# Optimization experiments

Hardware: AMD Instinct MI355X
Metric: run time of the kernel (lower is better)

The kernel has to match this reference:

```python
import jax, jax.numpy as jnp
import numpy as np

N_NODES = 50000
N_EDGES = 500000
HIDDEN = 64
NUM_BASIS = 32
NUM_SH = 4  # (lmax+1)^2 with lmax=1


def _mlp(x, w1, b1, w2, b2):
    # Linear -> SiLU -> Linear, matching nn.Sequential(Linear, SiLU, Linear)
    return jax.nn.silu(x @ w1 + b1) @ w2 + b2


def setup_inputs() -> dict:
    key = jax.random.key(0)
    ks = jax.random.split(key, 10)
    scale_in = 1.0 / np.sqrt(NUM_BASIS)
    scale_h = 1.0 / np.sqrt(HIDDEN)
    return {
        "scalar": jax.random.normal(ks[0], (N_NODES, HIDDEN), dtype=jnp.float32),
        "vector": jax.random.normal(ks[1], (N_NODES, 3, HIDDEN), dtype=jnp.float32),
        "edge_sh": jax.random.normal(ks[2], (N_EDGES, NUM_SH), dtype=jnp.float32),
        "edge_length": jax.random.uniform(ks[3], (N_EDGES, NUM_BASIS), dtype=jnp.float32),
        "edge_index": jax.random.randint(ks[4], (2, N_EDGES), 0, N_NODES, dtype=jnp.int32),
        "sw1": jax.random.normal(ks[5], (NUM_BASIS, HIDDEN), dtype=jnp.float32) * scale_in,
        "sb1": jnp.zeros((HIDDEN,), dtype=jnp.float32),
        "sw2": jax.random.normal(ks[6], (HIDDEN, HIDDEN), dtype=jnp.float32) * scale_h,
        "sb2": jnp.zeros((HIDDEN,), dtype=jnp.float32),
        "vw1": jax.random.normal(ks[7], (NUM_BASIS, HIDDEN), dtype=jnp.float32) * scale_in,
        "vb1": jnp.zeros((HIDDEN,), dtype=jnp.float32),
        "vw2": jax.random.normal(ks[8], (HIDDEN, HIDDEN), dtype=jnp.float32) * scale_h,
        "vb2": jnp.zeros((HIDDEN,), dtype=jnp.float32),
    }


def reference(scalar, vector, edge_sh, edge_length, edge_index,
              sw1, sb1, sw2, sb2, vw1, vb1, vw2, vb2):
    # edge_sh is accepted (as in the torch forward signature) but unused.
    row, col = edge_index[0], edge_index[1]
    n = scalar.shape[0]

    # Edge-wise MLP weights from radial basis expansion: [E, hidden]
    scalar_weights = _mlp(edge_length, sw1, sb1, sw2, sb2)
    # Gather source-node scalars, weight, scatter-add to destination nodes.
    scalar_msg = scalar[col] * scalar_weights                   # [E, hidden]
    out_scalar = jax.ops.segment_sum(scalar_msg, row, num_segments=n)

    vector_weights = _mlp(edge_length, vw1, vb1, vw2, vb2)      # [E, hidden]
    vector_msg = vector[col] * vector_weights[:, None, :]       # [E, 3, hidden]
    out_vector = jax.ops.segment_sum(vector_msg, row, num_segments=n)

    return out_scalar, out_vector
```

## Files before the change

kernel.cpp:

```cpp
#include <hip/hip_runtime.h>

#define HIDDEN 64
#define NB 32
#define SCAN_BLOCK 1024
#define HSTR 72

typedef __attribute__((ext_vector_type(8))) short bf16x8;
typedef __attribute__((ext_vector_type(4))) float f32x4;

static __device__ __forceinline__ unsigned short f2bf(float x) {
    union { float f; unsigned u; } v; v.f = x;
    unsigned r = v.u + 0x7fffu + ((v.u >> 16) & 1u);
    return (unsigned short)(r >> 16);
}
static __device__ __forceinline__ float bf2f(unsigned short s) {
    union { unsigned u; float f; } v; v.u = ((unsigned)s) << 16;
    return v.f;
}

__global__ __launch_bounds__(256) void hist_kernel(
    const int* __restrict__ edge_index, int* __restrict__ counts, int E)
{
    int i = blockIdx.x * 256 + threadIdx.x;
    if (i < E) atomicAdd(&counts[edge_index[i]], 1);
}

__global__ __launch_bounds__(SCAN_BLOCK) void scan_pass1(
    const int* __restrict__ counts, int* __restrict__ partial,
    int* __restrict__ blocksums, int N)
{
    __shared__ int tmp[SCAN_BLOCK];
    const int t = threadIdx.x;
    const int gid = blockIdx.x * SCAN_BLOCK + t;
    int v = (gid < N) ? counts[gid] : 0;
    tmp[t] = v;
    __syncthreads();
    for (int off = 1; off < SCAN_BLOCK; off <<= 1) {
        int x = (t >= off) ? tmp[t - off] : 0;
        __syncthreads();
        tmp[t] += x;
        __syncthreads();
    }
    if (gid < N) partial[gid] = tmp[t] - v;
    if (t == SCAN_BLOCK - 1) blocksums[blockIdx.x] = tmp[t];
}

__global__ void scan_pass2(int* __restrict__ blocksums, int nb)
{
    if (threadIdx.x == 0) {
        int acc = 0;
        for (int i = 0; i < nb; ++i) { int v = blocksums[i]; blocksums[i] = acc; acc += v; }
    }
}

__global__ __launch_bounds__(SCAN_BLOCK) void scan_pass3(
    const int* __restrict__ partial, const int* __restrict__ blocksums,
    int* __restrict__ offsets, int* __restrict__ cursors, int N, int E)
{
    const int gid = blockIdx.x * SCAN_BLOCK + threadIdx.x;
    if (gid < N) {
        int o = partial[gid] + blocksums[blockIdx.x];
        offsets[gid] = o;
        cursors[gid] = o;
    }
    if (blockIdx.x == 0 && threadIdx.x == 0) offsets[N] = E;
}

__global__ __launch_bounds__(256) void scatter_kernel(
    const int* __restrict__ edge_index, int* __restrict__ cursors,
    int* __restrict__ perm, int* __restrict__ perm_col, int E)
{
    int i = blockIdx.x * 256 + threadIdx.x;
    if (i < E) {
        int pos = atomicAdd(&cursors[edge_index[i]], 1);
        perm[pos] = i;
        perm_col[pos] = edge_index[E + i];
    }
}

__global__ __launch_bounds__(256) void mlp_mfma_kernel(
    const float* __restrict__ edge_length,
    const int*   __restrict__ perm,
    const float* __restrict__ sw1, const float* __restrict__ sb1,
    const float* __restrict__ sw2, const float* __restrict__ sb2,
    const float* __restrict__ vw1, const float* __restrict__ vb1,
    const float* __restrict__ vw2, const float* __restrict__ vb2,
    unsigned short* __restrict__ Ws,
    unsigned short* __restrict__ Wv,
    int E, int nchunks)
{
    __shared__ short Hs[4][64 * HSTR];

    const int t    = threadIdx.x;
    const int lane = t & 63;
    const int wid  = t >> 6;
    const int quad = lane >> 4;
    const int l16  = lane & 15;
    short* Hw = Hs[wid];

    const float* w1p[2] = {sw1, vw1};
    const float* b1p[2] = {sb1, vb1};
    const float* w2p[2] = {sw2, vw2};
    const float* b2p[2] = {sb2, vb2};
    unsigned short* outp[2] = {Ws, Wv};

    bf16x8 w1f[2][4];
    bf16x8 w2f[2][2][4];
    float  b1v[2][4], b2v[2][4];
    #pragma unroll
    for (int m = 0; m < 2; ++m) {
        #pragma unroll
        for (int nt = 0; nt < 4; ++nt) {
            const int col = nt * 16 + l16;
            #pragma unroll
            for (int j = 0; j < 8; ++j)
                w1f[m][nt][j] = (short)f2bf(w1p[m][(quad * 8 + j) * HIDDEN + col]);
            #pragma unroll
            for (int kk = 0; kk < 2; ++kk) {
                #pragma unroll
                for (int j = 0; j < 8; ++j)
                    w2f[m][kk][nt][j] = (short)f2bf(w2p[m][(kk * 32 + quad * 8 + j) * HIDDEN + col]);
            }
            b1v[m][nt] = b1p[m][col];
            b2v[m][nt] = b2p[m][col];
        }
    }

    const int wave_g = blockIdx.x * 4 + wid;
    const int nwaves = gridDim.x * 4;

    for (int c = wave_g; c < nchunks; c += nwaves) {
        const int j0 = c * 64;

        bf16x8 af[4];
        #pragma unroll
        for (int mt = 0; mt < 4; ++mt) {
            int j = j0 + mt * 16 + l16;
            int e = perm[j < E ? j : (E - 1)];
            const float* r = edge_length + (size_t)e * NB + quad * 8;
            float4 u0 = *(const float4*)r;
            float4 u1 = *(const float4*)(r + 4);
            af[mt][0] = (short)f2bf(u0.x); af[mt][1] = (short)f2bf(u0.y);
            af[mt][2] = (short)f2bf(u0.z); af[mt][3] = (short)f2bf(u0.w);
            af[mt][4] = (short)f2bf(u1.x); af[mt][5] = (short)f2bf(u1.y);
            af[mt][6] = (short)f2bf(u1.z); af[mt][7] = (short)f2bf(u1.w);
        }

        #pragma unroll
        for (int m = 0; m < 2; ++m) {
            #pragma unroll
            for (int mt = 0; mt < 4; ++mt) {
                #pragma unroll
                for (int nt = 0; nt < 4; ++nt) {
                    f32x4 cf = {b1v[m][nt], b1v[m][nt], b1v[m][nt], b1v[m][nt]};
                    cf = __builtin_amdgcn_mfma_f32_16x16x32_bf16(af[mt], w1f[m][nt], cf, 0, 0, 0);
                    #pragma unroll
                    for (int r4 = 0; r4 < 4; ++r4) {
                        float x = cf[r4];
                        x = x / (1.0f + __expf(-x));
                        const int row = mt * 16 + quad * 4 + r4;
                        Hw[row * HSTR + nt * 16 + l16] = (short)f2bf(x);
                    }
                }
            }

            #pragma unroll
            for (int mt = 0; mt < 4; ++mt) {
                const int arow = mt * 16 + l16;
                bf16x8 a0 = *(const bf16x8*)(Hw + arow * HSTR + quad * 8);
                bf16x8 a1 = *(const bf16x8*)(Hw + arow * HSTR + 32 + quad * 8);
                #pragma unroll
                for (int nt = 0; nt < 4; ++nt) {
                    f32x4 cf = {b2v[m][nt], b2v[m][nt], b2v[m][nt], b2v[m][nt]};
                    cf = __builtin_amdgcn_mfma_f32_16x16x32_bf16(a1, w2f[m][1][nt], cf, 0, 0, 0);
                    cf = __builtin_amdgcn_mfma_f32_16x16x32_bf16(a0, w2f[m][0][nt], cf, 0, 0, 0);
                    #pragma unroll
                    for (int r4 = 0; r4 < 4; ++r4) {
                        const int row = mt * 16 + quad * 4 + r4;
                        Hw[row * HSTR + nt * 16 + l16] = (short)f2bf(cf[r4]);
                    }
                }
            }

            unsigned short* op = outp[m] + (size_t)j0 * HIDDEN;
            #pragma unroll
            for (int i = 0; i < 8; ++i) {
                const int row = i * 8 + (lane >> 3);
                bf16x8 v = *(const bf16x8*)(Hw + row * HSTR + (lane & 7) * 8);
                if (j0 + row < E)
                    *(bf16x8*)(op + (size_t)i * 512 + lane * 8) = v;
            }
        }
    }
}

__global__ __launch_bounds__(256) void node_kernel(
    const float* __restrict__ scalar,
    const float* __restrict__ vector,
    const int* __restrict__ offsets,
    const int* __restrict__ perm_col,
    const unsigned short* __restrict__ Ws,
    const unsigned short* __restrict__ Wv,
    float* __restrict__ out_scalar,
    float* __restrict__ out_vector,
    int N)
{
    const int lane = threadIdx.x & 63;
    const int wave = blockIdx.x * 4 + (threadIdx.x >> 6);
    const int nw   = gridDim.x * 4;

    for (int n = wave; n < N; n += nw) {
        const int beg = offsets[n];
        const int end = offsets[n + 1];

        float as = 0.0f, a0 = 0.0f, a1 = 0.0f, a2 = 0.0f;

        for (int j = beg; j < end; ++j) {
            const int col = perm_col[j];
            const float w_s = bf2f(Ws[(size_t)j * HIDDEN + lane]);
            const float w_v = bf2f(Wv[(size_t)j * HIDDEN + lane]);
            const float* sp = scalar + (size_t)col * HIDDEN;
            const float* vp = vector + (size_t)col * 3 * HIDDEN;
            as = fmaf(sp[lane],       w_s, as);
            a0 = fmaf(vp[lane],       w_v, a0);
            a1 = fmaf(vp[64 + lane],  w_v, a1);
            a2 = fmaf(vp[128 + lane], w_v, a2);
        }

        out_scalar[(size_t)n * HIDDEN + lane] = as;
        float* ov = out_vector + (size_t)n * 3 * HIDDEN;
        ov[lane]       = a0;
        ov[64 + lane]  = a1;
        ov[128 + lane] = a2;
    }
}

extern "C" void kernel_launch(void* const* d_in, const int* in_sizes, int n_in,
                              void* d_out, int out_size, void* d_ws, size_t ws_size,
                              hipStream_t stream) {
    const float* scalar      = (const float*)d_in[0];
    const float* vector      = (const float*)d_in[1];
    const float* edge_length = (const float*)d_in[3];
    const int*   edge_index  = (const int*)d_in[4];
    const float* sw1 = (const float*)d_in[5];
    const float* sb1 = (const float*)d_in[6];
    const float* sw2 = (const float*)d_in[7];
    const float* sb2 = (const float*)d_in[8];
    const float* vw1 = (const float*)d_in[9];
    const float* vb1 = (const float*)d_in[10];
    const float* vw2 = (const float*)d_in[11];
    const float* vb2 = (const float*)d_in[12];

    const int N = in_sizes[0] / HIDDEN;
    const int E = in_sizes[4] / 2;

    float* out_scalar = (float*)d_out;
    float* out_vector = (float*)d_out + (size_t)N * HIDDEN;

    unsigned short* Ws = (unsigned short*)d_ws;
    unsigned short* Wv = Ws + (size_t)E * HIDDEN;
    int* ib = (int*)((char*)d_ws + (size_t)E * HIDDEN * 2 * 2);
    int* counts    = ib;
    int* partial   = ib + N;
    int* offsets   = ib + 2 * N;
    int* cursors   = ib + 3 * N + 1;
    int* blocksums = ib + 4 * N + 1;
    int* perm      = ib + 4 * N + 1 + 64;
    int* perm_col  = perm + E;

    hipMemsetAsync(counts, 0, (size_t)N * sizeof(int), stream);

    const int egrid = (E + 255) / 256;
    hist_kernel<<<egrid, 256, 0, stream>>>(edge_index, counts, E);

    const int nb = (N + SCAN_BLOCK - 1) / SCAN_BLOCK;
    scan_pass1<<<nb, SCAN_BLOCK, 0, stream>>>(counts, partial, blocksums, N);
    scan_pass2<<<1, 64, 0, stream>>>(blocksums, nb);
    scan_pass3<<<nb, SCAN_BLOCK, 0, stream>>>(partial, blocksums, offsets, cursors, N, E);

    scatter_kernel<<<egrid, 256, 0, stream>>>(edge_index, cursors, perm, perm_col, E);

    const int nchunks = (E + 63) / 64;
    mlp_mfma_kernel<<<512, 256, 0, stream>>>(
        edge_length, perm,
        sw1, sb1, sw2, sb2, vw1, vb1, vw2, vb2,
        Ws, Wv, E, nchunks);

    const int ngrid = (N + 3) / 4;
    node_kernel<<<ngrid, 256, 0, stream>>>(
        scalar, vector, offsets, perm_col, Ws, Wv,
        out_scalar, out_vector, N);
}
```

Baseline: 375.9 us.

## Run edge MLP in original order, interleave weights, single-block CSR scan, prefetch node loop

The edge MLP now processes edges in their original order, so edge_length reads are coalesced and no longer gathered through a permutation. Scalar and vector weights are stored interleaved per edge, and the node kernel fetches them by original edge id through a packed (edge, col) int2 array. The three-pass scan becomes one 1024-thread kernel, and the node loop software-prefetches the next edge's operands to overlap latency. The cost is that weight reads in the node kernel become random gathers of 256-byte rows instead of sequential reads.

```diff
diff --git a/kernel.cpp b/kernel.cpp
--- a/kernel.cpp
+++ b/kernel.cpp
@@ -2,7 +2,6 @@
 
 #define HIDDEN 64
 #define NB 32
-#define SCAN_BLOCK 1024
 #define HSTR 72
 
 typedef __attribute__((ext_vector_type(8))) short bf16x8;
@@ -25,68 +24,58 @@
     if (i < E) atomicAdd(&counts[edge_index[i]], 1);
 }
 
-__global__ __launch_bounds__(SCAN_BLOCK) void scan_pass1(
-    const int* __restrict__ counts, int* __restrict__ partial,
-    int* __restrict__ blocksums, int N)
-{
-    __shared__ int tmp[SCAN_BLOCK];
+__global__ __launch_bounds__(1024) void csr_scan_kernel(
+    const int* __restrict__ counts, int* __restrict__ offsets,
+    int* __restrict__ cursors, int N, int E)
+{
+    __shared__ int sums[1024];
     const int t = threadIdx.x;
-    const int gid = blockIdx.x * SCAN_BLOCK + t;
-    int v = (gid < N) ? counts[gid] : 0;
-    tmp[t] = v;
+    const int CH = (N + 1023) / 1024;
+    const int base = t * CH;
+
+    int s = 0;
+    for (int i = 0; i < CH; ++i) {
+        int idx = base + i;
+        if (idx < N) s += counts[idx];
+    }
+    sums[t] = s;
     __syncthreads();
-    for (int off = 1; off < SCAN_BLOCK; off <<= 1) {
-        int x = (t >= off) ? tmp[t - off] : 0;
+    for (int off = 1; off < 1024; off <<= 1) {
+        int x = (t >= off) ? sums[t - off] : 0;
         __syncthreads();
-        tmp[t] += x;
+        sums[t] += x;
         __syncthreads();
     }
-    if (gid < N) partial[gid] = tmp[t] - v;
-    if (t == SCAN_BLOCK - 1) blocksums[blockIdx.x] = tmp[t];
-}
-
-__global__ void scan_pass2(int* __restrict__ blocksums, int nb)
-{
-    if (threadIdx.x == 0) {
-        int acc = 0;
-        for (int i = 0; i < nb; ++i) { int v = blocksums[i]; blocksums[i] = acc; acc += v; }
-    }
-}
-
-__global__ __launch_bounds__(SCAN_BLOCK) void scan_pass3(
-    const int* __restrict__ partial, const int* __restrict__ blocksums,
-    int* __restrict__ offsets, int* __restrict__ cursors, int N, int E)
-{
-    const int gid = blockIdx.x * SCAN_BLOCK + threadIdx.x;
-    if (gid < N) {
-        int o = partial[gid] + blocksums[blockIdx.x];
-        offsets[gid] = o;
-        cursors[gid] = o;
-    }
-    if (blockIdx.x == 0 && threadIdx.x == 0) offsets[N] = E;
+    int run = sums[t] - s;
+    for (int i = 0; i < CH; ++i) {
+        int idx = base + i;
+        if (idx < N) {
+            offsets[idx] = run;
+            cursors[idx] = run;
+            run += counts[idx];
+        }
+    }
+    if (t == 0) offsets[N] = E;
 }
 
 __global__ __launch_bounds__(256) void scatter_kernel(
     const int* __restrict__ edge_index, int* __restrict__ cursors,
-    int* __restrict__ perm, int* __restrict__ perm_col, int E)
+    int2* __restrict__ pc, int E)
 {
     int i = blockIdx.x * 256 + threadIdx.x;
     if (i < E) {
         int pos = atomicAdd(&cursors[edge_index[i]], 1);
-        perm[pos] = i;
-        perm_col[pos] = edge_index[E + i];
+        pc[pos] = make_int2(i, edge_index[E + i]);
     }
 }
 
 __global__ __launch_bounds__(256) void mlp_mfma_kernel(
     const float* __restrict__ edge_length,
-    const int*   __restrict__ perm,
     const float* __restrict__ sw1, const float* __restrict__ sb1,
     const float* __restrict__ sw2, const float* __restrict__ sb2,
     const float* __restrict__ vw1, const float* __restrict__ vb1,
     const float* __restrict__ vw2, const float* __restrict__ vb2,
-    unsigned short* __restrict__ Ws,
-    unsigned short* __restrict__ Wv,
+    unsigned short* __restrict__ W,
     int E, int nchunks)
 {
     __shared__ short Hs[4][64 * HSTR];
@@ -102,7 +91,6 @@
     const float* b1p[2] = {sb1, vb1};
     const float* w2p[2] = {sw2, vw2};
     const float* b2p[2] = {sb2, vb2};
-    unsigned short* outp[2] = {Ws, Wv};
 
     bf16x8 w1f[2][4];
     bf16x8 w2f[2][2][4];
@@ -135,8 +123,8 @@
         bf16x8 af[4];
         #pragma unroll
         for (int mt = 0; mt < 4; ++mt) {
-            int j = j0 + mt * 16 + l16;
-            int e = perm[j < E ? j : (E - 1)];
+            int e = j0 + mt * 16 + l16;
+            if (e >= E) e = E - 1;
             const float* r = edge_length + (size_t)e * NB + quad * 8;
             float4 u0 = *(const float4*)r;
             float4 u1 = *(const float4*)(r + 4);
@@ -182,13 +170,12 @@
                 }
             }
 
-            unsigned short* op = outp[m] + (size_t)j0 * HIDDEN;
             #pragma unroll
             for (int i = 0; i < 8; ++i) {
                 const int row = i * 8 + (lane >> 3);
                 bf16x8 v = *(const bf16x8*)(Hw + row * HSTR + (lane & 7) * 8);
                 if (j0 + row < E)
-                    *(bf16x8*)(op + (size_t)i * 512 + lane * 8) = v;
+                    *(bf16x8*)(W + (size_t)(j0 + row) * 128 + m * 64 + (lane & 7) * 8) = v;
             }
         }
     }
@@ -198,9 +185,8 @@
     const float* __restrict__ scalar,
     const float* __restrict__ vector,
     const int* __restrict__ offsets,
-    const int* __restrict__ perm_col,
-    const unsigned short* __restrict__ Ws,
-    const unsigned short* __restrict__ Wv,
+    const int2* __restrict__ pc,
+    const unsigned short* __restrict__ W,
     float* __restrict__ out_scalar,
     float* __restrict__ out_vector,
     int N)
@@ -215,16 +201,35 @@
 
         float as = 0.0f, a0 = 0.0f, a1 = 0.0f, a2 = 0.0f;
 
+        float ws = 0, wv = 0, s = 0, v0 = 0, v1 = 0, v2 = 0;
+        if (beg < end) {
+            const int2 p = pc[beg];
+            const unsigned short* wp = W + (size_t)p.x * 128;
+            ws = bf2f(wp[lane]); wv = bf2f(wp[64 + lane]);
+            const float* sp = scalar + (size_t)p.y * HIDDEN;
+            const float* vp = vector + (size_t)p.y * 3 * HIDDEN;
+            s = sp[lane]; v0 = vp[lane]; v1 = vp[64 + lane]; v2 = vp[128 + lane];
+        }
+
         for (int j = beg; j < end; ++j) {
-            const int col = perm_col[j];
-            const float w_s = bf2f(Ws[(size_t)j * HIDDEN + lane]);
-            const float w_v = bf2f(Wv[(size_t)j * HIDDEN + lane]);
-            const float* sp = scalar + (size_t)col * HIDDEN;
-            const float* vp = vector + (size_t)col * 3 * HIDDEN;
-            as = fmaf(sp[lane],       w_s, as);
-            a0 = fmaf(vp[lane],       w_v, a0);
-            a1 = fmaf(vp[64 + lane],  w_v, a1);
-            a2 = fmaf(vp[128 + lane], w_v, a2);
+            const int jn = (j + 1 < end) ? j + 1 : j;
+            const int2 p = pc[jn];
+            const unsigned short* wp = W + (size_t)p.x * 128;
+            const float wsn = bf2f(wp[lane]);
+            const float wvn = bf2f(wp[64 + lane]);
+            const float* sp = scalar + (size_t)p.y * HIDDEN;
+            const float* vp = vector + (size_t)p.y * 3 * HIDDEN;
+            const float sn  = sp[lane];
+            const float v0n = vp[lane];
+            const float v1n = vp[64 + lane];
+            const float v2n = vp[128 + lane];
+
+            as = fmaf(s,  ws, as);
+            a0 = fmaf(v0, wv, a0);
+            a1 = fmaf(v1, wv, a1);
+            a2 = fmaf(v2, wv, a2);
+
+            ws = wsn; wv = wvn; s = sn; v0 = v0n; v1 = v1n; v2 = v2n;
         }
 
         out_scalar[(size_t)n * HIDDEN + lane] = as;
@@ -257,37 +262,29 @@
     float* out_scalar = (float*)d_out;
     float* out_vector = (float*)d_out + (size_t)N * HIDDEN;
 
-    unsigned short* Ws = (unsigned short*)d_ws;
-    unsigned short* Wv = Ws + (size_t)E * HIDDEN;
-    int* ib = (int*)((char*)d_ws + (size_t)E * HIDDEN * 2 * 2);
-    int* counts    = ib;
-    int* partial   = ib + N;
-    int* offsets   = ib + 2 * N;
-    int* cursors   = ib + 3 * N + 1;
-    int* blocksums = ib + 4 * N + 1;
-    int* perm      = ib + 4 * N + 1 + 64;
-    int* perm_col  = perm + E;
+    unsigned short* W = (unsigned short*)d_ws;
+    int* ib = (int*)((char*)d_ws + (size_t)E * 128 * 2);
+    int* counts  = ib;
+    int* offsets = ib + N;
+    int* cursors = ib + 2 * N + 1;
+    int2* pc     = (int2*)(ib + 3 * N + 2);
 
     hipMemsetAsync(counts, 0, (size_t)N * sizeof(int), stream);
 
     const int egrid = (E + 255) / 256;
-    hist_kernel<<<egrid, 256, 0, stream>>>(edge_index, counts, E);
-
-    const int nb = (N + SCAN_BLOCK - 1) / SCAN_BLOCK;
-    scan_pass1<<<nb, SCAN_BLOCK, 0, stream>>>(counts, partial, blocksums, N);
-    scan_pass2<<<1, 64, 0, stream>>>(blocksums, nb);
-    scan_pass3<<<nb, SCAN_BLOCK, 0, stream>>>(partial, blocksums, offsets, cursors, N, E);
-
-    scatter_kernel<<<egrid, 256, 0, stream>>>(edge_index, cursors, perm, perm_col, E);
 
     const int nchunks = (E + 63) / 64;
     mlp_mfma_kernel<<<512, 256, 0, stream>>>(
-        edge_length, perm,
+        edge_length,
         sw1, sb1, sw2, sb2, vw1, vb1, vw2, vb2,
-        Ws, Wv, E, nchunks);
+        W, E, nchunks);
+
+    hist_kernel<<<egrid, 256, 0, stream>>>(edge_index, counts, E);
+    csr_scan_kernel<<<1, 1024, 0, stream>>>(counts, offsets, cursors, N, E);
+    scatter_kernel<<<egrid, 256, 0, stream>>>(edge_index, cursors, pc, E);
 
     const int ngrid = (N + 3) / 4;
     node_kernel<<<ngrid, 256, 0, stream>>>(
-        scalar, vector, offsets, perm_col, Ws, Wv,
+        scalar, vector, offsets, pc, W,
         out_scalar, out_vector, N);
 }
```

Result: slower. 478.6 us (+27.3%).

## Pack node features to bf16, fuse histogram into MLP, interleave edge data

Applied to the files above, without the earlier changes.

Adds a pre-pass that packs scalar and vector node features into one bf16 ushort4 array, so each gathered neighbour needs a single 8-byte load per lane instead of four fp32 loads. The histogram is folded into the MLP kernel, which now runs in original edge order and writes both weight sets interleaved per edge. The scatter writes a combined (edge, col) int2 record, the block-sum scan uses wave shuffles, and the node loop prefetches the next edge. Risks are added bf16 rounding of node features, weights now read in unsorted edge order (less locality), and a fallback path when the workspace is too small.

```diff
diff --git a/kernel.cpp b/kernel.cpp
--- a/kernel.cpp
+++ b/kernel.cpp
@@ -18,11 +18,22 @@
     return v.f;
 }
 
-__global__ __launch_bounds__(256) void hist_kernel(
-    const int* __restrict__ edge_index, int* __restrict__ counts, int E)
+__global__ __launch_bounds__(256) void featpack_kernel(
+    const float* __restrict__ scalar,
+    const float* __restrict__ vector,
+    ushort4* __restrict__ feat,
+    int total)
 {
     int i = blockIdx.x * 256 + threadIdx.x;
-    if (i < E) atomicAdd(&counts[edge_index[i]], 1);
+    if (i >= total) return;
+    const int n = i >> 6, l = i & 63;
+    const float* vp = vector + (size_t)n * 192 + l;
+    ushort4 o;
+    o.x = f2bf(scalar[i]);
+    o.y = f2bf(vp[0]);
+    o.z = f2bf(vp[64]);
+    o.w = f2bf(vp[128]);
+    feat[i] = o;
 }
 
 __global__ __launch_bounds__(SCAN_BLOCK) void scan_pass1(
@@ -45,12 +56,17 @@
     if (t == SCAN_BLOCK - 1) blocksums[blockIdx.x] = tmp[t];
 }
 
-__global__ void scan_pass2(int* __restrict__ blocksums, int nb)
-{
-    if (threadIdx.x == 0) {
-        int acc = 0;
-        for (int i = 0; i < nb; ++i) { int v = blocksums[i]; blocksums[i] = acc; acc += v; }
-    }
+__global__ __launch_bounds__(64) void scan_pass2(int* __restrict__ blocksums, int nb)
+{
+    const int t = threadIdx.x;
+    int v = (t < nb) ? blocksums[t] : 0;
+    int s = v;
+    #pragma unroll
+    for (int off = 1; off < 64; off <<= 1) {
+        int x = __shfl_up(s, off, 64);
+        if (t >= off) s += x;
+    }
+    if (t < nb) blocksums[t] = s - v;
 }
 
 __global__ __launch_bounds__(SCAN_BLOCK) void scan_pass3(
@@ -68,25 +84,24 @@
 
 __global__ __launch_bounds__(256) void scatter_kernel(
     const int* __restrict__ edge_index, int* __restrict__ cursors,
-    int* __restrict__ perm, int* __restrict__ perm_col, int E)
+    int2* __restrict__ pc, int E)
 {
     int i = blockIdx.x * 256 + threadIdx.x;
     if (i < E) {
         int pos = atomicAdd(&cursors[edge_index[i]], 1);
-        perm[pos] = i;
-        perm_col[pos] = edge_index[E + i];
+        pc[pos] = make_int2(i, edge_index[E + i]);
     }
 }
 
 __global__ __launch_bounds__(256) void mlp_mfma_kernel(
     const float* __restrict__ edge_length,
-    const int*   __restrict__ perm,
+    const int*   __restrict__ edge_index,
+    int* __restrict__ counts,
     const float* __restrict__ sw1, const float* __restrict__ sb1,
     const float* __restrict__ sw2, const float* __restrict__ sb2,
     const float* __restrict__ vw1, const float* __restrict__ vb1,
     const float* __restrict__ vw2, const float* __restrict__ vb2,
-    unsigned short* __restrict__ Ws,
-    unsigned short* __restrict__ Wv,
+    unsigned short* __restrict__ W,
     int E, int nchunks)
 {
     __shared__ short Hs[4][64 * HSTR];
@@ -102,7 +117,6 @@
     const float* b1p[2] = {sb1, vb1};
     const float* w2p[2] = {sw2, vw2};
     const float* b2p[2] = {sb2, vb2};
-    unsigned short* outp[2] = {Ws, Wv};
 
     bf16x8 w1f[2][4];
     bf16x8 w2f[2][2][4];
@@ -132,11 +146,16 @@
     for (int c = wave_g; c < nchunks; c += nwaves) {
         const int j0 = c * 64;
 
+        {
+            const int e = j0 + lane;
+            if (e < E) atomicAdd(&counts[edge_index[e]], 1);
+        }
+
         bf16x8 af[4];
         #pragma unroll
         for (int mt = 0; mt < 4; ++mt) {
-            int j = j0 + mt * 16 + l16;
-            int e = perm[j < E ? j : (E - 1)];
+            int e = j0 + mt * 16 + l16;
+            if (e >= E) e = E - 1;
             const float* r = edge_length + (size_t)e * NB + quad * 8;
             float4 u0 = *(const float4*)r;
             float4 u1 = *(const float4*)(r + 4);
@@ -182,25 +201,79 @@
                 }
             }
 
-            unsigned short* op = outp[m] + (size_t)j0 * HIDDEN;
             #pragma unroll
             for (int i = 0; i < 8; ++i) {
                 const int row = i * 8 + (lane >> 3);
                 bf16x8 v = *(const bf16x8*)(Hw + row * HSTR + (lane & 7) * 8);
                 if (j0 + row < E)
-                    *(bf16x8*)(op + (size_t)i * 512 + lane * 8) = v;
+                    *(bf16x8*)(W + (size_t)(j0 + row) * 128 + m * 64 + (lane & 7) * 8) = v;
             }
         }
     }
 }
 
-__global__ __launch_bounds__(256) void node_kernel(
+__global__ __launch_bounds__(256) void node_kernel_feat(
+    const ushort4* __restrict__ feat,
+    const int* __restrict__ offsets,
+    const int2* __restrict__ pc,
+    const unsigned short* __restrict__ W,
+    float* __restrict__ out_scalar,
+    float* __restrict__ out_vector,
+    int N)
+{
+    const int lane = threadIdx.x & 63;
+    const int wave = blockIdx.x * 4 + (threadIdx.x >> 6);
+    const int nw   = gridDim.x * 4;
+
+    for (int n = wave; n < N; n += nw) {
+        const int beg = offsets[n];
+        const int end = offsets[n + 1];
+
+        float as = 0.0f, a0 = 0.0f, a1 = 0.0f, a2 = 0.0f;
+        float ws = 0, wv = 0, s = 0, v0 = 0, v1 = 0, v2 = 0;
+
+        if (beg < end) {
+            const int2 p = pc[beg];
+            const unsigned short* wp = W + (size_t)p.x * 128;
+            ws = bf2f(wp[lane]); wv = bf2f(wp[64 + lane]);
+            const ushort4 f = feat[(size_t)p.y * 64 + lane];
+            s = bf2f(f.x); v0 = bf2f(f.y); v1 = bf2f(f.z); v2 = bf2f(f.w);
+        }
+
+        for (int j = beg; j < end; ++j) {
+            const int jn = (j + 1 < end) ? j + 1 : j;
+            const int2 p = pc[jn];
+            const unsigned short* wp = W + (size_t)p.x * 128;
+            const float wsn = bf2f(wp[lane]);
+            const float wvn = bf2f(wp[64 + lane]);
+            const ushort4 f = feat[(size_t)p.y * 64 + lane];
+            const float sn  = bf2f(f.x);
+            const float v0n = bf2f(f.y);
+            const float v1n = bf2f(f.z);
+            const float v2n = bf2f(f.w);
+
+            as = fmaf(s,  ws, as);
+            a0 = fmaf(v0, wv, a0);
+            a1 = fmaf(v1, wv, a1);
+            a2 = fmaf(v2, wv, a2);
+
+            ws = wsn; wv = wvn; s = sn; v0 = v0n; v1 = v1n; v2 = v2n;
+        }
+
+        out_scalar[(size_t)n * HIDDEN + lane] = as;
+        float* ov = out_vector + (size_t)n * 3 * HIDDEN;
+        ov[lane]       = a0;
+        ov[64 + lane]  = a1;
+        ov[128 + lane] = a2;
+    }
+}
+
+__global__ __launch_bounds__(256) void node_kernel_f32(
     const float* __restrict__ scalar,
     const float* __restrict__ vector,
     const int* __restrict__ offsets,
-    const int* __restrict__ perm_col,
-    const unsigned short* __restrict__ Ws,
-    const unsigned short* __restrict__ Wv,
+    const int2* __restrict__ pc,
+    const unsigned short* __restrict__ W,
     float* __restrict__ out_scalar,
     float* __restrict__ out_vector,
     int N)
@@ -212,21 +285,19 @@
     for (int n = wave; n < N; n += nw) {
         const int beg = offsets[n];
         const int end = offsets[n + 1];
-
         float as = 0.0f, a0 = 0.0f, a1 = 0.0f, a2 = 0.0f;
-
         for (int j = beg; j < end; ++j) {
-            const int col = perm_col[j];
-            const float w_s = bf2f(Ws[(size_t)j * HIDDEN + lane]);
-            const float w_v = bf2f(Wv[(size_t)j * HIDDEN + lane]);
-            const float* sp = scalar + (size_t)col * HIDDEN;
-            const float* vp = vector + (size_t)col * 3 * HIDDEN;
+            const int2 p = pc[j];
+            const unsigned short* wp = W + (size_t)p.x * 128;
+            const float w_s = bf2f(wp[lane]);
+            const float w_v = bf2f(wp[64 + lane]);
+            const float* sp = scalar + (size_t)p.y * HIDDEN;
+            const float* vp = vector + (size_t)p.y * 3 * HIDDEN;
             as = fmaf(sp[lane],       w_s, as);
             a0 = fmaf(vp[lane],       w_v, a0);
             a1 = fmaf(vp[64 + lane],  w_v, a1);
             a2 = fmaf(vp[128 + lane], w_v, a2);
         }
-
         out_scalar[(size_t)n * HIDDEN + lane] = as;
         float* ov = out_vector + (size_t)n * 3 * HIDDEN;
         ov[lane]       = a0;
@@ -257,37 +328,50 @@
     float* out_scalar = (float*)d_out;
     float* out_vector = (float*)d_out + (size_t)N * HIDDEN;
 
-    unsigned short* Ws = (unsigned short*)d_ws;
-    unsigned short* Wv = Ws + (size_t)E * HIDDEN;
-    int* ib = (int*)((char*)d_ws + (size_t)E * HIDDEN * 2 * 2);
+    size_t off = 0;
+    unsigned short* W = (unsigned short*)d_ws;
+    off += (size_t)E * 128 * 2;
+    int2* pc = (int2*)((char*)d_ws + off);
+    off += (size_t)E * 8;
+    int* ib = (int*)((char*)d_ws + off);
     int* counts    = ib;
     int* partial   = ib + N;
     int* offsets   = ib + 2 * N;
     int* cursors   = ib + 3 * N + 1;
     int* blocksums = ib + 4 * N + 1;
-    int* perm      = ib + 4 * N + 1 + 64;
-    int* perm_col  = perm + E;
+    off += ((size_t)4 * N + 1 + 64) * 4;
+    off = (off + 15) & ~(size_t)15;
+    ushort4* feat = (ushort4*)((char*)d_ws + off);
+    const bool use_feat = (off + (size_t)N * 64 * 8) <= ws_size;
 
     hipMemsetAsync(counts, 0, (size_t)N * sizeof(int), stream);
 
     const int egrid = (E + 255) / 256;
-    hist_kernel<<<egrid, 256, 0, stream>>>(edge_index, counts, E);
+
+    if (use_feat) {
+        const int total = N * 64;
+        featpack_kernel<<<(total + 255) / 256, 256, 0, stream>>>(
+            scalar, vector, feat, total);
+    }
+
+    const int nchunks = (E + 63) / 64;
+    mlp_mfma_kernel<<<512, 256, 0, stream>>>(
+        edge_length, edge_index, counts,
+        sw1, sb1, sw2, sb2, vw1, vb1, vw2, vb2,
+        W, E, nchunks);
 
     const int nb = (N + SCAN_BLOCK - 1) / SCAN_BLOCK;
     scan_pass1<<<nb, SCAN_BLOCK, 0, stream>>>(counts, partial, blocksums, N);
     scan_pass2<<<1, 64, 0, stream>>>(blocksums, nb);
     scan_pass3<<<nb, SCAN_BLOCK, 0, stream>>>(partial, blocksums, offsets, cursors, N, E);
-
-    scatter_kernel<<<egrid, 256, 0, stream>>>(edge_index, cursors, perm, perm_col, E);
-
-    const int nchunks = (E + 63) / 64;
-    mlp_mfma_kernel<<<512, 256, 0, stream>>>(
-        edge_length, perm,
-        sw1, sb1, sw2, sb2, vw1, vb1, vw2, vb2,
-        Ws, Wv, E, nchunks);
+    scatter_kernel<<<egrid, 256, 0, stream>>>(edge_index, cursors, pc, E);
 
     const int ngrid = (N + 3) / 4;
-    node_kernel<<<ngrid, 256, 0, stream>>>(
-        scalar, vector, offsets, perm_col, Ws, Wv,
-        out_scalar, out_vector, N);
-}
+    if (use_feat) {
+        node_kernel_feat<<<ngrid, 256, 0, stream>>>(
+            feat, offsets, pc, W, out_scalar, out_vector, N);
+    } else {
+        node_kernel_f32<<<ngrid, 256, 0, stream>>>(
+            scalar, vector, offsets, pc, W, out_scalar, out_vector, N);
+    }
+}
```

Result: faster. 335.4 us (-10.8%).
